# Kernel tuning notes

Measured on AMD Instinct MI355X. Metric: run time of the kernel, lower is better.

Reference implementation:

```python
import jax, jax.numpy as jnp
import numpy as np

N_WIRES = 4
N_ENT_LAYERS = 2  # params per hybrid layer have shape (2, 4)


def apply_rx(state, theta, wire):
    """Apply RX(theta) on `wire`. state: (B,2,2,2,2) complex64; theta: scalar or (B,)."""
    half = theta * 0.5
    c = jnp.cos(half).astype(jnp.complex64)
    s = (-1j) * jnp.sin(half).astype(jnp.complex64)
    moved = jnp.moveaxis(state, 1 + wire, -1)  # (B, 2,2,2, 2)
    a0, a1 = moved[..., 0], moved[..., 1]      # (B, 2,2,2)
    c = c.reshape(c.shape + (1,) * (a0.ndim - c.ndim))
    s = s.reshape(s.shape + (1,) * (a0.ndim - s.ndim))
    new = jnp.stack([c * a0 + s * a1, s * a0 + c * a1], axis=-1)
    return jnp.moveaxis(new, -1, 1 + wire)


def apply_cnot(state, control, target):
    s = jnp.moveaxis(state, [1 + control, 1 + target], [-2, -1])  # (..., 2c, 2t)
    new = jnp.stack([s[..., 0, :], s[..., 1, ::-1]], axis=-2)      # flip target where control=1
    return jnp.moveaxis(new, [-2, -1], [1 + control, 1 + target])


def expvals_z(state):
    probs = state.real ** 2 + state.imag ** 2  # (B,2,2,2,2)
    outs = []
    for w in range(N_WIRES):
        p = jnp.moveaxis(probs, 1 + w, 1)
        outs.append(jnp.sum(p[:, 0] - p[:, 1], axis=(1, 2, 3)))
    return jnp.stack(outs, axis=-1)  # (B, 4)


def qnn_batch(angles, layer_params):
    """angles: (B,4) float; layer_params: (2,4) float. Returns (B,4) Z expvals."""
    B = angles.shape[0]
    state = jnp.zeros((B,) + (2,) * N_WIRES, dtype=jnp.complex64)
    state = state.at[(slice(None),) + (0,) * N_WIRES].set(1.0)
    # AngleEmbedding (RX rotations)
    for w in range(N_WIRES):
        state = apply_rx(state, angles[:, w], w)
    # BasicEntanglerLayers: RX per wire then CNOT ring
    for l in range(N_ENT_LAYERS):
        for w in range(N_WIRES):
            state = apply_rx(state, layer_params[l, w], w)
        for w in range(N_WIRES):
            state = apply_cnot(state, w, (w + 1) % N_WIRES)
    return expvals_z(state)


def setup_inputs() -> dict:
    key = jax.random.key(0)
    ks = jax.random.split(key, 8)
    B, D_IN = 524288, 16
    inp = {
        "x": jax.random.normal(ks[0], (B, D_IN), dtype=jnp.float32),
        "theta": jax.random.normal(ks[1], (3, 2, 4), dtype=jnp.float32) * 0.01,
        "W0": jax.random.normal(ks[2], (D_IN, 4), dtype=jnp.float32) / np.sqrt(D_IN),
        "b0": jnp.zeros((4,), dtype=jnp.float32),
        "W1": jax.random.normal(ks[3], (4, 4), dtype=jnp.float32) / 2.0,
        "b1": jnp.zeros((4,), dtype=jnp.float32),
        "W2": jax.random.normal(ks[4], (4, 4), dtype=jnp.float32) / 2.0,
        "b2": jnp.zeros((4,), dtype=jnp.float32),
    }
    return inp


def reference(x, theta, W0, b0, W1, b1, W2, b2):
    Ws = [(W0, b0), (W1, b1), (W2, b2)]
    h = x
    for i, (W, b) in enumerate(Ws):
        h = jnp.tanh(h @ W + b)        # Dense + tanh
        h = qnn_batch(h, theta[i])      # vmapped 4-qubit circuit
        # Dropout(rate=0, deterministic=True) is identity
    return h
```

## Files before the change

### kernel.cpp

```cpp
#include <hip/hip_runtime.h>
#include <math.h>


__device__ __forceinline__ float fast_tanh(float x) {
    float u = __expf(2.0f * x);
    return 1.0f - 2.0f * __builtin_amdgcn_rcpf(u + 1.0f);
}


__device__ __forceinline__ void s_apply_rx(float2 st[16], int w, float c, float s) {
    const int bit = 1 << w;
#pragma unroll
    for (int b = 0; b < 16; ++b) {
        if (!(b & bit)) {
            float2 a0 = st[b];
            float2 a1 = st[b | bit];
            st[b].x       = fmaf(c, a0.x,  s * a1.y);
            st[b].y       = fmaf(c, a0.y, -s * a1.x);
            st[b | bit].x = fmaf(c, a1.x,  s * a0.y);
            st[b | bit].y = fmaf(c, a1.y, -s * a0.x);
        }
    }
}

__device__ __forceinline__ void s_apply_cnot(float2 st[16], int c, int t) {
    const int cb = 1 << c, tb = 1 << t;
#pragma unroll
    for (int b = 0; b < 16; ++b) {
        if ((b & cb) && !(b & tb)) {
            float2 tmp = st[b];
            st[b] = st[b | tb];
            st[b | tb] = tmp;
        }
    }
}

__global__ void setup_D(const float* __restrict__ theta, float* __restrict__ D) {
    __shared__ float bufA[81 * 4];
    __shared__ float bufB[81 * 4];
    const int t = threadIdx.x;

    for (int layer = 0; layer < 3; ++layer) {
        if (t < 81) {
            const int g0 = t % 3, g1 = (t / 3) % 3, g2 = (t / 9) % 3, g3 = t / 27;
            const float H[3] = {0.0f, 1.5707963267948966f, 3.14159265358979323f};
            float h[4] = {H[g0], H[g1], H[g2], H[g3]};

            float2 st[16];
#pragma unroll
            for (int b = 0; b < 16; ++b) st[b] = make_float2(0.0f, 0.0f);
            st[0] = make_float2(1.0f, 0.0f);

            for (int w = 0; w < 4; ++w)
                s_apply_rx(st, w, cosf(0.5f * h[w]), sinf(0.5f * h[w]));
            for (int l = 0; l < 2; ++l) {
                for (int w = 0; w < 4; ++w) {
                    float th = 0.5f * theta[layer * 8 + l * 4 + w];
                    s_apply_rx(st, w, cosf(th), sinf(th));
                }
                for (int w = 0; w < 4; ++w)
                    s_apply_cnot(st, w, (w + 1) & 3);
            }
            float pr[16], total = 0.0f;
#pragma unroll
            for (int b = 0; b < 16; ++b) {
                pr[b] = st[b].x * st[b].x + st[b].y * st[b].y;
                total += pr[b];
            }
            for (int w = 0; w < 4; ++w) {
                float s1 = 0.0f;
#pragma unroll
                for (int b = 0; b < 16; ++b)
                    if ((b >> w) & 1) s1 += pr[b];
                bufA[t * 4 + w] = total - 2.0f * s1;
            }
        }
        __syncthreads();

        float* src = bufA;
        float* dst = bufB;
        int stride = 1;
        for (int d = 0; d < 4; ++d) {
            if (t < 81) {
                int digit = (t / stride) % 3;
                int base = t - digit * stride;
                for (int c = 0; c < 4; ++c) {
                    float y0 = src[(base + 0 * stride) * 4 + c];
                    float y1 = src[(base + 1 * stride) * 4 + c];
                    float y2 = src[(base + 2 * stride) * 4 + c];
                    float m = 0.5f * (y0 + y2);
                    float a = (digit == 0) ? m : (digit == 1) ? 0.5f * (y0 - y2) : (y1 - m);
                    dst[t * 4 + c] = a;
                }
            }
            __syncthreads();
            float* tmp = src; src = dst; dst = tmp;
            stride *= 3;
        }
        if (t < 81) {
            for (int c = 0; c < 4; ++c)
                D[(layer * 81 + t) * 4 + c] = src[t * 4 + c];
        }
        __syncthreads();
    }
}


__global__ __launch_bounds__(256, 4)
void hqnn_kernel(const float4* __restrict__ x4,
                 const float4* __restrict__ D4,
                 const float* __restrict__ W0, const float* __restrict__ b0,
                 const float* __restrict__ W1, const float* __restrict__ b1,
                 const float* __restrict__ W2, const float* __restrict__ b2,
                 float4* __restrict__ out, int B) {
    int i = blockIdx.x * blockDim.x + threadIdx.x;
    if (i >= B) return;

    float4 v0 = x4[i * 4 + 0];
    float4 v1 = x4[i * 4 + 1];
    float4 v2 = x4[i * 4 + 2];
    float4 v3 = x4[i * 4 + 3];
    float xr[16] = {v0.x, v0.y, v0.z, v0.w, v1.x, v1.y, v1.z, v1.w,
                    v2.x, v2.y, v2.z, v2.w, v3.x, v3.y, v3.z, v3.w};

    float h[4];
#pragma unroll
    for (int j = 0; j < 4; ++j) {
        float acc = b0[j];
#pragma unroll
        for (int k = 0; k < 16; ++k) acc = fmaf(xr[k], W0[k * 4 + j], acc);
        h[j] = fast_tanh(acc);
    }

#pragma unroll
    for (int layer = 0; layer < 3; ++layer) {
        if (layer > 0) {
            const float* W = (layer == 1) ? W1 : W2;
            const float* b = (layer == 1) ? b1 : b2;
            float g[4];
#pragma unroll
            for (int j = 0; j < 4; ++j) {
                float acc = b[j];
#pragma unroll
                for (int k = 0; k < 4; ++k) acc = fmaf(h[k], W[k * 4 + j], acc);
                g[j] = fast_tanh(acc);
            }
#pragma unroll
            for (int j = 0; j < 4; ++j) h[j] = g[j];
        }

        float c0 = __cosf(h[0]), s0 = __sinf(h[0]);
        float c1 = __cosf(h[1]), s1 = __sinf(h[1]);
        float c2 = __cosf(h[2]), s2 = __sinf(h[2]);
        float c3 = __cosf(h[3]), s3 = __sinf(h[3]);

        float p01[9] = {1.0f, c0, s0, c1, c1 * c0, c1 * s0, s1, s1 * c0, s1 * s0};
        float p23[9] = {1.0f, c2, s2, c3, c3 * c2, c3 * s2, s3, s3 * c2, s3 * s2};

        float E0 = 0.0f, E1 = 0.0f, E2 = 0.0f, E3 = 0.0f;
#pragma unroll
        for (int j = 0; j < 9; ++j) {
#pragma unroll
            for (int ii = 0; ii < 9; ++ii) {
                float T = p01[ii] * p23[j];
                float4 d = D4[layer * 81 + j * 9 + ii];
                E0 = fmaf(d.x, T, E0);
                E1 = fmaf(d.y, T, E1);
                E2 = fmaf(d.z, T, E2);
                E3 = fmaf(d.w, T, E3);
            }
        }
        h[0] = E0; h[1] = E1; h[2] = E2; h[3] = E3;
    }

    out[i] = make_float4(h[0], h[1], h[2], h[3]);
}

extern "C" void kernel_launch(void* const* d_in, const int* in_sizes, int n_in,
                              void* d_out, int out_size, void* d_ws, size_t ws_size,
                              hipStream_t stream) {
    const float* x  = (const float*)d_in[0];
    const float* th = (const float*)d_in[1];
    const float* W0 = (const float*)d_in[2];
    const float* b0 = (const float*)d_in[3];
    const float* W1 = (const float*)d_in[4];
    const float* b1 = (const float*)d_in[5];
    const float* W2 = (const float*)d_in[6];
    const float* b2 = (const float*)d_in[7];
    float* out = (float*)d_out;
    float* D   = (float*)d_ws;

    int B = in_sizes[0] / 16;

    hipLaunchKernelGGL(setup_D, dim3(1), dim3(128), 0, stream, th, D);

    int block = 256;
    int grid = (B + block - 1) / block;
    hipLaunchKernelGGL(hqnn_kernel, dim3(grid), dim3(block), 0, stream,
                       (const float4*)x, (const float4*)D,
                       W0, b0, W1, b1, W2, b2,
                       (float4*)out, B);
}
```

Before: 121.6 us.

## Process two rows per thread with packed FMA and parallelize setup across layers

The main kernel now handles two batch rows per thread (rows i and i+Bhalf). Each D4 coefficient load is shared between both rows, and the accumulation uses 2-wide vector types so the compiler can emit packed FP32 FMAs. The setup kernel launches one block per layer instead of looping over three layers in a single block, and it switches to fast sin and cos intrinsics. The cost is higher register pressure. The code also assumes an even B, since an odd B would leave one row unprocessed.

```diff
diff --git a/kernel.cpp b/kernel.cpp
--- a/kernel.cpp
+++ b/kernel.cpp
@@ -1,6 +1,8 @@
 #include <hip/hip_runtime.h>
 #include <math.h>
 
+
+typedef float v2f __attribute__((ext_vector_type(2)));
 
 __device__ __forceinline__ float fast_tanh(float x) {
     float u = __expf(2.0f * x);
@@ -39,72 +41,115 @@
     __shared__ float bufA[81 * 4];
     __shared__ float bufB[81 * 4];
     const int t = threadIdx.x;
-
-    for (int layer = 0; layer < 3; ++layer) {
+    const int layer = blockIdx.x;
+
+    if (t < 81) {
+        const int g0 = t % 3, g1 = (t / 3) % 3, g2 = (t / 9) % 3, g3 = t / 27;
+        const float H[3] = {0.0f, 1.5707963267948966f, 3.14159265358979323f};
+        float h[4] = {H[g0], H[g1], H[g2], H[g3]};
+
+        float2 st[16];
+#pragma unroll
+        for (int b = 0; b < 16; ++b) st[b] = make_float2(0.0f, 0.0f);
+        st[0] = make_float2(1.0f, 0.0f);
+
+        for (int w = 0; w < 4; ++w)
+            s_apply_rx(st, w, __cosf(0.5f * h[w]), __sinf(0.5f * h[w]));
+        for (int l = 0; l < 2; ++l) {
+            for (int w = 0; w < 4; ++w) {
+                float th = 0.5f * theta[layer * 8 + l * 4 + w];
+                s_apply_rx(st, w, __cosf(th), __sinf(th));
+            }
+            for (int w = 0; w < 4; ++w)
+                s_apply_cnot(st, w, (w + 1) & 3);
+        }
+        float pr[16], total = 0.0f;
+#pragma unroll
+        for (int b = 0; b < 16; ++b) {
+            pr[b] = st[b].x * st[b].x + st[b].y * st[b].y;
+            total += pr[b];
+        }
+        for (int w = 0; w < 4; ++w) {
+            float s1 = 0.0f;
+#pragma unroll
+            for (int b = 0; b < 16; ++b)
+                if ((b >> w) & 1) s1 += pr[b];
+            bufA[t * 4 + w] = total - 2.0f * s1;
+        }
+    }
+    __syncthreads();
+
+    float* src = bufA;
+    float* dst = bufB;
+    int stride = 1;
+    for (int d = 0; d < 4; ++d) {
         if (t < 81) {
-            const int g0 = t % 3, g1 = (t / 3) % 3, g2 = (t / 9) % 3, g3 = t / 27;
-            const float H[3] = {0.0f, 1.5707963267948966f, 3.14159265358979323f};
-            float h[4] = {H[g0], H[g1], H[g2], H[g3]};
-
-            float2 st[16];
-#pragma unroll
-            for (int b = 0; b < 16; ++b) st[b] = make_float2(0.0f, 0.0f);
-            st[0] = make_float2(1.0f, 0.0f);
-
-            for (int w = 0; w < 4; ++w)
-                s_apply_rx(st, w, cosf(0.5f * h[w]), sinf(0.5f * h[w]));
-            for (int l = 0; l < 2; ++l) {
-                for (int w = 0; w < 4; ++w) {
-                    float th = 0.5f * theta[layer * 8 + l * 4 + w];
-                    s_apply_rx(st, w, cosf(th), sinf(th));
-                }
-                for (int w = 0; w < 4; ++w)
-                    s_apply_cnot(st, w, (w + 1) & 3);
+            int digit = (t / stride) % 3;
+            int base = t - digit * stride;
+            for (int c = 0; c < 4; ++c) {
+                float y0 = src[(base + 0 * stride) * 4 + c];
+                float y1 = src[(base + 1 * stride) * 4 + c];
+                float y2 = src[(base + 2 * stride) * 4 + c];
+                float m = 0.5f * (y0 + y2);
+                float a = (digit == 0) ? m : (digit == 1) ? 0.5f * (y0 - y2) : (y1 - m);
+                dst[t * 4 + c] = a;
             }
-            float pr[16], total = 0.0f;
-#pragma unroll
-            for (int b = 0; b < 16; ++b) {
-                pr[b] = st[b].x * st[b].x + st[b].y * st[b].y;
-                total += pr[b];
-            }
-            for (int w = 0; w < 4; ++w) {
-                float s1 = 0.0f;
-#pragma unroll
-                for (int b = 0; b < 16; ++b)
-                    if ((b >> w) & 1) s1 += pr[b];
-                bufA[t * 4 + w] = total - 2.0f * s1;
-            }
         }
         __syncthreads();
-
-        float* src = bufA;
-        float* dst = bufB;
-        int stride = 1;
-        for (int d = 0; d < 4; ++d) {
-            if (t < 81) {
-                int digit = (t / stride) % 3;
-                int base = t - digit * stride;
-                for (int c = 0; c < 4; ++c) {
-                    float y0 = src[(base + 0 * stride) * 4 + c];
-                    float y1 = src[(base + 1 * stride) * 4 + c];
-                    float y2 = src[(base + 2 * stride) * 4 + c];
-                    float m = 0.5f * (y0 + y2);
-                    float a = (digit == 0) ? m : (digit == 1) ? 0.5f * (y0 - y2) : (y1 - m);
-                    dst[t * 4 + c] = a;
-                }
-            }
-            __syncthreads();
-            float* tmp = src; src = dst; dst = tmp;
-            stride *= 3;
-        }
-        if (t < 81) {
-            for (int c = 0; c < 4; ++c)
-                D[(layer * 81 + t) * 4 + c] = src[t * 4 + c];
-        }
-        __syncthreads();
-    }
-}
-
+        float* tmp = src; src = dst; dst = tmp;
+        stride *= 3;
+    }
+    if (t < 81) {
+        for (int c = 0; c < 4; ++c)
+            D[(layer * 81 + t) * 4 + c] = src[t * 4 + c];
+    }
+}
+
+
+__device__ __forceinline__ void dense_tanh4(float h[4], const float* __restrict__ W,
+                                            const float* __restrict__ b) {
+    float g[4];
+#pragma unroll
+    for (int j = 0; j < 4; ++j) {
+        float acc = b[j];
+#pragma unroll
+        for (int k = 0; k < 4; ++k) acc = fmaf(h[k], W[k * 4 + j], acc);
+        g[j] = fast_tanh(acc);
+    }
+#pragma unroll
+    for (int j = 0; j < 4; ++j) h[j] = g[j];
+}
+
+__device__ __forceinline__ void dense0_tanh(const float4* __restrict__ x4, int row,
+                                            const float* __restrict__ W0,
+                                            const float* __restrict__ b0, float h[4]) {
+    float4 v0 = x4[row * 4 + 0];
+    float4 v1 = x4[row * 4 + 1];
+    float4 v2 = x4[row * 4 + 2];
+    float4 v3 = x4[row * 4 + 3];
+    float xr[16] = {v0.x, v0.y, v0.z, v0.w, v1.x, v1.y, v1.z, v1.w,
+                    v2.x, v2.y, v2.z, v2.w, v3.x, v3.y, v3.z, v3.w};
+#pragma unroll
+    for (int j = 0; j < 4; ++j) {
+        float acc = b0[j];
+#pragma unroll
+        for (int k = 0; k < 16; ++k) acc = fmaf(xr[k], W0[k * 4 + j], acc);
+        h[j] = fast_tanh(acc);
+    }
+}
+
+__device__ __forceinline__ void build_tables(const float h[4], float p01[9], float p23[9]) {
+    float c0 = __cosf(h[0]), s0 = __sinf(h[0]);
+    float c1 = __cosf(h[1]), s1 = __sinf(h[1]);
+    float c2 = __cosf(h[2]), s2 = __sinf(h[2]);
+    float c3 = __cosf(h[3]), s3 = __sinf(h[3]);
+    p01[0] = 1.0f; p01[1] = c0;      p01[2] = s0;
+    p01[3] = c1;   p01[4] = c1 * c0; p01[5] = c1 * s0;
+    p01[6] = s1;   p01[7] = s1 * c0; p01[8] = s1 * s0;
+    p23[0] = 1.0f; p23[1] = c2;      p23[2] = s2;
+    p23[3] = c3;   p23[4] = c3 * c2; p23[5] = c3 * s2;
+    p23[6] = s3;   p23[7] = s3 * c2; p23[8] = s3 * s2;
+}
 
 __global__ __launch_bounds__(256, 4)
 void hqnn_kernel(const float4* __restrict__ x4,
@@ -112,68 +157,53 @@
                  const float* __restrict__ W0, const float* __restrict__ b0,
                  const float* __restrict__ W1, const float* __restrict__ b1,
                  const float* __restrict__ W2, const float* __restrict__ b2,
-                 float4* __restrict__ out, int B) {
+                 float4* __restrict__ out, int Bhalf) {
     int i = blockIdx.x * blockDim.x + threadIdx.x;
-    if (i >= B) return;
-
-    float4 v0 = x4[i * 4 + 0];
-    float4 v1 = x4[i * 4 + 1];
-    float4 v2 = x4[i * 4 + 2];
-    float4 v3 = x4[i * 4 + 3];
-    float xr[16] = {v0.x, v0.y, v0.z, v0.w, v1.x, v1.y, v1.z, v1.w,
-                    v2.x, v2.y, v2.z, v2.w, v3.x, v3.y, v3.z, v3.w};
-
-    float h[4];
-#pragma unroll
-    for (int j = 0; j < 4; ++j) {
-        float acc = b0[j];
-#pragma unroll
-        for (int k = 0; k < 16; ++k) acc = fmaf(xr[k], W0[k * 4 + j], acc);
-        h[j] = fast_tanh(acc);
-    }
+    if (i >= Bhalf) return;
+    const int ra = i, rb = i + Bhalf;
+
+    float ha[4], hb[4];
+    dense0_tanh(x4, ra, W0, b0, ha);
+    dense0_tanh(x4, rb, W0, b0, hb);
 
 #pragma unroll
     for (int layer = 0; layer < 3; ++layer) {
         if (layer > 0) {
             const float* W = (layer == 1) ? W1 : W2;
             const float* b = (layer == 1) ? b1 : b2;
-            float g[4];
-#pragma unroll
-            for (int j = 0; j < 4; ++j) {
-                float acc = b[j];
-#pragma unroll
-                for (int k = 0; k < 4; ++k) acc = fmaf(h[k], W[k * 4 + j], acc);
-                g[j] = fast_tanh(acc);
+            dense_tanh4(ha, W, b);
+            dense_tanh4(hb, W, b);
+        }
+
+        float p01a[9], p23a[9], p01b[9], p23b[9];
+        build_tables(ha, p01a, p23a);
+        build_tables(hb, p01b, p23b);
+
+        v2f Ea01 = {0.0f, 0.0f}, Ea23 = {0.0f, 0.0f};
+        v2f Eb01 = {0.0f, 0.0f}, Eb23 = {0.0f, 0.0f};
+#pragma unroll
+        for (int j = 0; j < 9; ++j) {
+#pragma unroll
+            for (int ii = 0; ii < 9; ++ii) {
+                float4 d = D4[layer * 81 + j * 9 + ii];
+                v2f d01 = {d.x, d.y};
+                v2f d23 = {d.z, d.w};
+                float Ta = p01a[ii] * p23a[j];
+                float Tb = p01b[ii] * p23b[j];
+                v2f Tva = {Ta, Ta};
+                v2f Tvb = {Tb, Tb};
+                Ea01 = d01 * Tva + Ea01;
+                Ea23 = d23 * Tva + Ea23;
+                Eb01 = d01 * Tvb + Eb01;
+                Eb23 = d23 * Tvb + Eb23;
             }
-#pragma unroll
-            for (int j = 0; j < 4; ++j) h[j] = g[j];
-        }
-
-        float c0 = __cosf(h[0]), s0 = __sinf(h[0]);
-        float c1 = __cosf(h[1]), s1 = __sinf(h[1]);
-        float c2 = __cosf(h[2]), s2 = __sinf(h[2]);
-        float c3 = __cosf(h[3]), s3 = __sinf(h[3]);
-
-        float p01[9] = {1.0f, c0, s0, c1, c1 * c0, c1 * s0, s1, s1 * c0, s1 * s0};
-        float p23[9] = {1.0f, c2, s2, c3, c3 * c2, c3 * s2, s3, s3 * c2, s3 * s2};
-
-        float E0 = 0.0f, E1 = 0.0f, E2 = 0.0f, E3 = 0.0f;
-#pragma unroll
-        for (int j = 0; j < 9; ++j) {
-#pragma unroll
-            for (int ii = 0; ii < 9; ++ii) {
-                float T = p01[ii] * p23[j];
-                float4 d = D4[layer * 81 + j * 9 + ii];
-                E0 = fmaf(d.x, T, E0);
-                E1 = fmaf(d.y, T, E1);
-                E2 = fmaf(d.z, T, E2);
-                E3 = fmaf(d.w, T, E3);
-            }
-        }
-        h[0] = E0; h[1] = E1; h[2] = E2; h[3] = E3;
-    }
-
-    out[i] = make_float4(h[0], h[1], h[2], h[3]);
+        }
+        ha[0] = Ea01.x; ha[1] = Ea01.y; ha[2] = Ea23.x; ha[3] = Ea23.y;
+        hb[0] = Eb01.x; hb[1] = Eb01.y; hb[2] = Eb23.x; hb[3] = Eb23.y;
+    }
+
+    out[ra] = make_float4(ha[0], ha[1], ha[2], ha[3]);
+    out[rb] = make_float4(hb[0], hb[1], hb[2], hb[3]);
 }
 
 extern "C" void kernel_launch(void* const* d_in, const int* in_sizes, int n_in,
@@ -191,13 +221,14 @@
     float* D   = (float*)d_ws;
 
     int B = in_sizes[0] / 16;
-
-    hipLaunchKernelGGL(setup_D, dim3(1), dim3(128), 0, stream, th, D);
+    int Bhalf = B / 2;
+
+    hipLaunchKernelGGL(setup_D, dim3(3), dim3(128), 0, stream, th, D);
 
     int block = 256;
-    int grid = (B + block - 1) / block;
+    int grid = (Bhalf + block - 1) / block;
     hipLaunchKernelGGL(hqnn_kernel, dim3(grid), dim3(block), 0, stream,
                        (const float4*)x, (const float4*)D,
                        W0, b0, W1, b1, W2, b2,
-                       (float4*)out, B);
-}
+                       (float4*)out, Bhalf);
+}
```

New measurement: 103.3 us. -15.0%, faster.

## Process two rows per thread with packed float2 math and parallelize setup

Applied to the files above, without the earlier changes.

The main kernel now handles two batch rows per thread (rows i and i+Bhalf) using 2-wide vector types, so the compiler can emit packed FMA instructions and each D coefficient load serves two rows. The setup kernel runs one block per layer instead of looping over three layers in a single block, and uses fast __cosf/__sinf. The cost is higher register pressure and half as many threads, which may reduce occupancy. An odd B would leave the last row uncomputed.

```diff
diff --git a/kernel.cpp b/kernel.cpp
--- a/kernel.cpp
+++ b/kernel.cpp
@@ -2,9 +2,15 @@
 #include <math.h>
 
 
-__device__ __forceinline__ float fast_tanh(float x) {
-    float u = __expf(2.0f * x);
-    return 1.0f - 2.0f * __builtin_amdgcn_rcpf(u + 1.0f);
+typedef float v2f __attribute__((ext_vector_type(2)));
+
+__device__ __forceinline__ v2f splat2(float x) { return (v2f){x, x}; }
+
+__device__ __forceinline__ v2f fast_tanh2(v2f x) {
+    float ua = __expf(2.0f * x.x);
+    float ub = __expf(2.0f * x.y);
+    v2f r = {__builtin_amdgcn_rcpf(ua + 1.0f), __builtin_amdgcn_rcpf(ub + 1.0f)};
+    return splat2(-2.0f) * r + splat2(1.0f);
 }
 
 
@@ -39,69 +45,67 @@
     __shared__ float bufA[81 * 4];
     __shared__ float bufB[81 * 4];
     const int t = threadIdx.x;
-
-    for (int layer = 0; layer < 3; ++layer) {
+    const int layer = blockIdx.x;
+
+    if (t < 81) {
+        const int g0 = t % 3, g1 = (t / 3) % 3, g2 = (t / 9) % 3, g3 = t / 27;
+        const float H[3] = {0.0f, 1.5707963267948966f, 3.14159265358979323f};
+        float h[4] = {H[g0], H[g1], H[g2], H[g3]};
+
+        float2 st[16];
+#pragma unroll
+        for (int b = 0; b < 16; ++b) st[b] = make_float2(0.0f, 0.0f);
+        st[0] = make_float2(1.0f, 0.0f);
+
+        for (int w = 0; w < 4; ++w)
+            s_apply_rx(st, w, __cosf(0.5f * h[w]), __sinf(0.5f * h[w]));
+        for (int l = 0; l < 2; ++l) {
+            for (int w = 0; w < 4; ++w) {
+                float th = 0.5f * theta[layer * 8 + l * 4 + w];
+                s_apply_rx(st, w, __cosf(th), __sinf(th));
+            }
+            for (int w = 0; w < 4; ++w)
+                s_apply_cnot(st, w, (w + 1) & 3);
+        }
+        float pr[16], total = 0.0f;
+#pragma unroll
+        for (int b = 0; b < 16; ++b) {
+            pr[b] = st[b].x * st[b].x + st[b].y * st[b].y;
+            total += pr[b];
+        }
+        for (int w = 0; w < 4; ++w) {
+            float s1 = 0.0f;
+#pragma unroll
+            for (int b = 0; b < 16; ++b)
+                if ((b >> w) & 1) s1 += pr[b];
+            bufA[t * 4 + w] = total - 2.0f * s1;
+        }
+    }
+    __syncthreads();
+
+    float* src = bufA;
+    float* dst = bufB;
+    int stride = 1;
+    for (int d = 0; d < 4; ++d) {
         if (t < 81) {
-            const int g0 = t % 3, g1 = (t / 3) % 3, g2 = (t / 9) % 3, g3 = t / 27;
-            const float H[3] = {0.0f, 1.5707963267948966f, 3.14159265358979323f};
-            float h[4] = {H[g0], H[g1], H[g2], H[g3]};
-
-            float2 st[16];
-#pragma unroll
-            for (int b = 0; b < 16; ++b) st[b] = make_float2(0.0f, 0.0f);
-            st[0] = make_float2(1.0f, 0.0f);
-
-            for (int w = 0; w < 4; ++w)
-                s_apply_rx(st, w, cosf(0.5f * h[w]), sinf(0.5f * h[w]));
-            for (int l = 0; l < 2; ++l) {
-                for (int w = 0; w < 4; ++w) {
-                    float th = 0.5f * theta[layer * 8 + l * 4 + w];
-                    s_apply_rx(st, w, cosf(th), sinf(th));
-                }
-                for (int w = 0; w < 4; ++w)
-                    s_apply_cnot(st, w, (w + 1) & 3);
-            }
-            float pr[16], total = 0.0f;
-#pragma unroll
-            for (int b = 0; b < 16; ++b) {
-                pr[b] = st[b].x * st[b].x + st[b].y * st[b].y;
-                total += pr[b];
-            }
-            for (int w = 0; w < 4; ++w) {
-                float s1 = 0.0f;
-#pragma unroll
-                for (int b = 0; b < 16; ++b)
-                    if ((b >> w) & 1) s1 += pr[b];
-                bufA[t * 4 + w] = total - 2.0f * s1;
+            int digit = (t / stride) % 3;
+            int base = t - digit * stride;
+            for (int c = 0; c < 4; ++c) {
+                float y0 = src[(base + 0 * stride) * 4 + c];
+                float y1 = src[(base + 1 * stride) * 4 + c];
+                float y2 = src[(base + 2 * stride) * 4 + c];
+                float m = 0.5f * (y0 + y2);
+                float a = (digit == 0) ? m : (digit == 1) ? 0.5f * (y0 - y2) : (y1 - m);
+                dst[t * 4 + c] = a;
             }
         }
         __syncthreads();
-
-        float* src = bufA;
-        float* dst = bufB;
-        int stride = 1;
-        for (int d = 0; d < 4; ++d) {
-            if (t < 81) {
-                int digit = (t / stride) % 3;
-                int base = t - digit * stride;
-                for (int c = 0; c < 4; ++c) {
-                    float y0 = src[(base + 0 * stride) * 4 + c];
-                    float y1 = src[(base + 1 * stride) * 4 + c];
-                    float y2 = src[(base + 2 * stride) * 4 + c];
-                    float m = 0.5f * (y0 + y2);
-                    float a = (digit == 0) ? m : (digit == 1) ? 0.5f * (y0 - y2) : (y1 - m);
-                    dst[t * 4 + c] = a;
-                }
-            }
-            __syncthreads();
-            float* tmp = src; src = dst; dst = tmp;
-            stride *= 3;
-        }
-        if (t < 81) {
-            for (int c = 0; c < 4; ++c)
-                D[(layer * 81 + t) * 4 + c] = src[t * 4 + c];
-        }
-        __syncthreads();
+        float* tmp = src; src = dst; dst = tmp;
+        stride *= 3;
+    }
+    if (t < 81) {
+        for (int c = 0; c < 4; ++c)
+            D[(layer * 81 + t) * 4 + c] = src[t * 4 + c];
     }
 }
 
@@ -112,68 +116,74 @@
                  const float* __restrict__ W0, const float* __restrict__ b0,
                  const float* __restrict__ W1, const float* __restrict__ b1,
                  const float* __restrict__ W2, const float* __restrict__ b2,
-                 float4* __restrict__ out, int B) {
+                 float4* __restrict__ out, int Bhalf) {
     int i = blockIdx.x * blockDim.x + threadIdx.x;
-    if (i >= B) return;
-
-    float4 v0 = x4[i * 4 + 0];
-    float4 v1 = x4[i * 4 + 1];
-    float4 v2 = x4[i * 4 + 2];
-    float4 v3 = x4[i * 4 + 3];
-    float xr[16] = {v0.x, v0.y, v0.z, v0.w, v1.x, v1.y, v1.z, v1.w,
-                    v2.x, v2.y, v2.z, v2.w, v3.x, v3.y, v3.z, v3.w};
-
-    float h[4];
+    if (i >= Bhalf) return;
+    const int ra = i, rb = i + Bhalf;
+
+    float4 a0 = x4[ra * 4 + 0], a1 = x4[ra * 4 + 1];
+    float4 a2 = x4[ra * 4 + 2], a3 = x4[ra * 4 + 3];
+    float4 bq0 = x4[rb * 4 + 0], bq1 = x4[rb * 4 + 1];
+    float4 bq2 = x4[rb * 4 + 2], bq3 = x4[rb * 4 + 3];
+    v2f xab[16] = {
+        {a0.x, bq0.x}, {a0.y, bq0.y}, {a0.z, bq0.z}, {a0.w, bq0.w},
+        {a1.x, bq1.x}, {a1.y, bq1.y}, {a1.z, bq1.z}, {a1.w, bq1.w},
+        {a2.x, bq2.x}, {a2.y, bq2.y}, {a2.z, bq2.z}, {a2.w, bq2.w},
+        {a3.x, bq3.x}, {a3.y, bq3.y}, {a3.z, bq3.z}, {a3.w, bq3.w}};
+
+    v2f h[4];
 #pragma unroll
     for (int j = 0; j < 4; ++j) {
-        float acc = b0[j];
-#pragma unroll
-        for (int k = 0; k < 16; ++k) acc = fmaf(xr[k], W0[k * 4 + j], acc);
-        h[j] = fast_tanh(acc);
+        v2f acc = splat2(b0[j]);
+#pragma unroll
+        for (int k = 0; k < 16; ++k)
+            acc = splat2(W0[k * 4 + j]) * xab[k] + acc;
+        h[j] = fast_tanh2(acc);
     }
 
 #pragma unroll
     for (int layer = 0; layer < 3; ++layer) {
-        if (layer > 0) {
-            const float* W = (layer == 1) ? W1 : W2;
-            const float* b = (layer == 1) ? b1 : b2;
-            float g[4];
+        v2f c0 = {__cosf(h[0].x), __cosf(h[0].y)}, s0 = {__sinf(h[0].x), __sinf(h[0].y)};
+        v2f c1 = {__cosf(h[1].x), __cosf(h[1].y)}, s1 = {__sinf(h[1].x), __sinf(h[1].y)};
+        v2f c2 = {__cosf(h[2].x), __cosf(h[2].y)}, s2 = {__sinf(h[2].x), __sinf(h[2].y)};
+        v2f c3 = {__cosf(h[3].x), __cosf(h[3].y)}, s3 = {__sinf(h[3].x), __sinf(h[3].y)};
+
+        v2f one = splat2(1.0f);
+        v2f p01[9] = {one, c0, s0, c1, c1 * c0, c1 * s0, s1, s1 * c0, s1 * s0};
+        v2f p23[9] = {one, c2, s2, c3, c3 * c2, c3 * s2, s3, s3 * c2, s3 * s2};
+
+        v2f E0 = {0.0f, 0.0f}, E1 = {0.0f, 0.0f};
+        v2f E2 = {0.0f, 0.0f}, E3 = {0.0f, 0.0f};
+#pragma unroll
+        for (int j = 0; j < 9; ++j) {
+#pragma unroll
+            for (int ii = 0; ii < 9; ++ii) {
+                float4 d = D4[layer * 81 + j * 9 + ii];
+                v2f T = p01[ii] * p23[j];
+                E0 = splat2(d.x) * T + E0;
+                E1 = splat2(d.y) * T + E1;
+                E2 = splat2(d.z) * T + E2;
+                E3 = splat2(d.w) * T + E3;
+            }
+        }
+
+        if (layer < 2) {
+            const float* W = (layer == 0) ? W1 : W2;
+            const float* bb = (layer == 0) ? b1 : b2;
+            v2f e[4] = {E0, E1, E2, E3};
 #pragma unroll
             for (int j = 0; j < 4; ++j) {
-                float acc = b[j];
-#pragma unroll
-                for (int k = 0; k < 4; ++k) acc = fmaf(h[k], W[k * 4 + j], acc);
-                g[j] = fast_tanh(acc);
-            }
-#pragma unroll
-            for (int j = 0; j < 4; ++j) h[j] = g[j];
-        }
-
-        float c0 = __cosf(h[0]), s0 = __sinf(h[0]);
-        float c1 = __cosf(h[1]), s1 = __sinf(h[1]);
-        float c2 = __cosf(h[2]), s2 = __sinf(h[2]);
-        float c3 = __cosf(h[3]), s3 = __sinf(h[3]);
-
-        float p01[9] = {1.0f, c0, s0, c1, c1 * c0, c1 * s0, s1, s1 * c0, s1 * s0};
-        float p23[9] = {1.0f, c2, s2, c3, c3 * c2, c3 * s2, s3, s3 * c2, s3 * s2};
-
-        float E0 = 0.0f, E1 = 0.0f, E2 = 0.0f, E3 = 0.0f;
-#pragma unroll
-        for (int j = 0; j < 9; ++j) {
-#pragma unroll
-            for (int ii = 0; ii < 9; ++ii) {
-                float T = p01[ii] * p23[j];
-                float4 d = D4[layer * 81 + j * 9 + ii];
-                E0 = fmaf(d.x, T, E0);
-                E1 = fmaf(d.y, T, E1);
-                E2 = fmaf(d.z, T, E2);
-                E3 = fmaf(d.w, T, E3);
-            }
-        }
-        h[0] = E0; h[1] = E1; h[2] = E2; h[3] = E3;
-    }
-
-    out[i] = make_float4(h[0], h[1], h[2], h[3]);
+                v2f acc = splat2(bb[j]);
+#pragma unroll
+                for (int k = 0; k < 4; ++k)
+                    acc = splat2(W[k * 4 + j]) * e[k] + acc;
+                h[j] = fast_tanh2(acc);
+            }
+        } else {
+            out[ra] = make_float4(E0.x, E1.x, E2.x, E3.x);
+            out[rb] = make_float4(E0.y, E1.y, E2.y, E3.y);
+        }
+    }
 }
 
 extern "C" void kernel_launch(void* const* d_in, const int* in_sizes, int n_in,
@@ -191,13 +201,14 @@
     float* D   = (float*)d_ws;
 
     int B = in_sizes[0] / 16;
-
-    hipLaunchKernelGGL(setup_D, dim3(1), dim3(128), 0, stream, th, D);
+    int Bhalf = B / 2;
+
+    hipLaunchKernelGGL(setup_D, dim3(3), dim3(128), 0, stream, th, D);
 
     int block = 256;
-    int grid = (B + block - 1) / block;
+    int grid = (Bhalf + block - 1) / block;
     hipLaunchKernelGGL(hqnn_kernel, dim3(grid), dim3(block), 0, stream,
                        (const float4*)x, (const float4*)D,
                        W0, b0, W1, b1, W2, b2,
-                       (float4*)out, B);
-}
+                       (float4*)out, Bhalf);
+}
```

Result: faster. 106.9 us (-12.1%).
